# Kernel optimization log

Hardware: AMD Instinct MI355X
Metric: run time of the kernel (lower is better)

## Reference

```python
import jax, jax.numpy as jnp
import numpy as np

C_CONST = 0.0  # polynomial kernel additive constant (init arg c)
D_CONST = 2    # polynomial kernel degree (init arg d)


def setup_inputs() -> dict:
    key = jax.random.key(0)
    k1, k2 = jax.random.split(key)
    input = jax.random.normal(k1, (1, 64, 128, 64), dtype=jnp.float32)
    target = jax.random.normal(k2, (1, 64, 128, 64), dtype=jnp.float32)
    return {"input": input, "target": target}


def reference(input, target):
    ch = input.shape[1]
    hw_input = input.shape[2] * input.shape[3]
    hw_target = target.shape[2] * target.shape[3]
    # Flatten to [hw, c] feature matrices (batch assumed 1, as in the original view(c, -1).T)
    F = input.reshape(ch, -1).T   # [hw_input, c]
    S = target.reshape(ch, -1).T  # [hw_target, c]

    def kernel(A, B):
        # Naive polynomial kernel Gram matrix: (A @ B^T + c)^d
        return (A @ B.T + C_CONST) ** D_CONST

    loss = kernel(F, F) + kernel(S, S) - 2.0 * kernel(F, S)
    return loss.sum() / hw_input / hw_target / (ch ** 2)
```

## Files before the change

### kernel.cpp

```cpp
#include <hip/hip_runtime.h>


#define CH    64
#define KTOT  8192
#define G1    256
#define KPB   (KTOT / G1)
#define KPG   (KPB / 2)

#define NORMF 3.637978807091713e-12f

__global__ __launch_bounds__(512, 4) void gram_partial(
    const float* __restrict__ in, const float* __restrict__ tg,
    float* __restrict__ ws, float* __restrict__ out)
{
    __shared__ __attribute__((aligned(16))) float ts_in[KPB][CH];
    __shared__ __attribute__((aligned(16))) float ts_tg[KPB][CH];
    __shared__ __attribute__((aligned(16))) float red[4096];

    const int t  = threadIdx.x;
    const int k0 = blockIdx.x * KPB;

    if (blockIdx.x == 0 && t == 0) out[0] = 0.f;

    {
        const int lch = t >> 3;
        const int lko = (t & 7) << 2;
        const float4 vi = *(const float4*)(in + lch * KTOT + k0 + lko);
        const float4 vt = *(const float4*)(tg + lch * KTOT + k0 + lko);
        ts_in[lko + 0][lch] = vi.x; ts_in[lko + 1][lch] = vi.y;
        ts_in[lko + 2][lch] = vi.z; ts_in[lko + 3][lch] = vi.w;
        ts_tg[lko + 0][lch] = vt.x; ts_tg[lko + 1][lch] = vt.y;
        ts_tg[lko + 2][lch] = vt.z; ts_tg[lko + 3][lch] = vt.w;
    }
    __syncthreads();

    const int g   = t >> 8;
    const int tid = t & 255;
    const int ty  = tid >> 4;
    const int tx  = tid & 15;
    const int a0  = ty << 2;
    const int b0  = tx << 2;

    float acc[4][4];
#pragma unroll
    for (int i = 0; i < 4; ++i)
#pragma unroll
        for (int j = 0; j < 4; ++j) acc[i][j] = 0.f;

#pragma unroll
    for (int kk = g * KPG; kk < g * KPG + KPG; ++kk) {
        const float4 av = *(const float4*)&ts_in[kk][a0];
        const float4 bv = *(const float4*)&ts_in[kk][b0];
        const float4 cv = *(const float4*)&ts_tg[kk][a0];
        const float4 dv = *(const float4*)&ts_tg[kk][b0];
        const float aa[4] = {av.x, av.y, av.z, av.w};
        const float bb[4] = {bv.x, bv.y, bv.z, bv.w};
        const float cc[4] = {cv.x, cv.y, cv.z, cv.w};
        const float dd[4] = {dv.x, dv.y, dv.z, dv.w};
#pragma unroll
        for (int i = 0; i < 4; ++i)
#pragma unroll
            for (int j = 0; j < 4; ++j) {
                acc[i][j] = fmaf(aa[i], bb[j], acc[i][j]);
                acc[i][j] = fmaf(-cc[i], dd[j], acc[i][j]);
            }
    }

    if (g == 1) {
#pragma unroll
        for (int i = 0; i < 4; ++i) {
            float4 v;
            v.x = acc[i][0]; v.y = acc[i][1]; v.z = acc[i][2]; v.w = acc[i][3];
            *(float4*)&red[tid * 16 + i * 4] = v;
        }
    }
    __syncthreads();
    if (g == 0) {
        float* p = ws + blockIdx.x * 4096;
#pragma unroll
        for (int i = 0; i < 4; ++i) {
            const float4 r = *(const float4*)&red[tid * 16 + i * 4];
            float4 v;
            v.x = acc[i][0] + r.x; v.y = acc[i][1] + r.y;
            v.z = acc[i][2] + r.z; v.w = acc[i][3] + r.w;
            *(float4*)(p + (a0 + i) * 64 + b0) = v;
        }
    }
}

__global__ __launch_bounds__(256) void reduce_square(
    const float* __restrict__ ws, float* __restrict__ out)
{
    __shared__ float red2[4][64];
    const int t  = threadIdx.x;
    const int el = t & 63;
    const int sl = t >> 6;
    const int e  = (blockIdx.x << 6) + el;

    float s = 0.f;
    const int p0 = sl * (G1 / 4);
#pragma unroll 16
    for (int p = p0; p < p0 + (G1 / 4); ++p)
        s += ws[p * 4096 + e];
    red2[sl][el] = s;
    __syncthreads();

    if (t < 64) {
        float tot = red2[0][t] + red2[1][t] + red2[2][t] + red2[3][t];
        float sq  = tot * tot;
#pragma unroll
        for (int off = 32; off > 0; off >>= 1)
            sq += __shfl_down(sq, off);
        if (t == 0) atomicAdd(out, sq * NORMF);
    }
}

extern "C" void kernel_launch(void* const* d_in, const int* in_sizes, int n_in,
                              void* d_out, int out_size, void* d_ws, size_t ws_size,
                              hipStream_t stream)
{
    const float* in = (const float*)d_in[0];
    const float* tg = (const float*)d_in[1];
    float* out = (float*)d_out;
    float* ws  = (float*)d_ws;

    gram_partial<<<G1, 512, 0, stream>>>(in, tg, ws, out);
    reduce_square<<<64, 256, 0, stream>>>(ws, out);
}
```

Before: 62.97 us.

## Use 8x8 register tiles per thread, 4-way K split, and wider reduction grid

The Gram partial kernel now runs 256 threads per block, with each thread computing an 8x8 tile instead of 4x4. Each of the four wavefronts handles 8 of the 32 k-rows, and pairs of wavefronts are combined through an XOR-swizzled shared buffer. This halves the threads per block and increases register reuse per LDS load. Each block now writes two partial 64x64 matrices, so the workspace doubles; the reduce kernel is relaunched with 256 blocks of 16 elements each to read these with more parallelism. The risks are higher register pressure, lower occupancy, and twice as much workspace traffic.

```diff
diff --git a/kernel.cpp b/kernel.cpp
--- a/kernel.cpp
+++ b/kernel.cpp
@@ -4,18 +4,22 @@
 #define CH    64
 #define KTOT  8192
 #define G1    256
-#define KPB   (KTOT / G1)
-#define KPG   (KPB / 2)
+#define KPB   32
+#define KPW   8
+#define NPART 2
+#define NP    (G1 * NPART)
 
 #define NORMF 3.637978807091713e-12f
 
-__global__ __launch_bounds__(512, 4) void gram_partial(
+#define RCOL(row, tb) ((tb) ^ ((row) & 56))
+
+__global__ __launch_bounds__(256, 1) void gram_partial(
     const float* __restrict__ in, const float* __restrict__ tg,
     float* __restrict__ ws, float* __restrict__ out)
 {
     __shared__ __attribute__((aligned(16))) float ts_in[KPB][CH];
     __shared__ __attribute__((aligned(16))) float ts_tg[KPB][CH];
-    __shared__ __attribute__((aligned(16))) float red[4096];
+    __shared__ __attribute__((aligned(16))) float red[2][CH][CH];
 
     const int t  = threadIdx.x;
     const int k0 = blockIdx.x * KPB;
@@ -23,67 +27,82 @@
     if (blockIdx.x == 0 && t == 0) out[0] = 0.f;
 
     {
-        const int lch = t >> 3;
-        const int lko = (t & 7) << 2;
-        const float4 vi = *(const float4*)(in + lch * KTOT + k0 + lko);
-        const float4 vt = *(const float4*)(tg + lch * KTOT + k0 + lko);
-        ts_in[lko + 0][lch] = vi.x; ts_in[lko + 1][lch] = vi.y;
-        ts_in[lko + 2][lch] = vi.z; ts_in[lko + 3][lch] = vi.w;
-        ts_tg[lko + 0][lch] = vt.x; ts_tg[lko + 1][lch] = vt.y;
-        ts_tg[lko + 2][lch] = vt.z; ts_tg[lko + 3][lch] = vt.w;
+        const int lk = (t & 7) << 2;
+#pragma unroll
+        for (int r = 0; r < 2; ++r) {
+            const int lch = (t >> 3) + 32 * r;
+            const float4 vi = *(const float4*)(in + lch * KTOT + k0 + lk);
+            const float4 vt = *(const float4*)(tg + lch * KTOT + k0 + lk);
+            ts_in[lk + 0][lch] = vi.x; ts_in[lk + 1][lch] = vi.y;
+            ts_in[lk + 2][lch] = vi.z; ts_in[lk + 3][lch] = vi.w;
+            ts_tg[lk + 0][lch] = vt.x; ts_tg[lk + 1][lch] = vt.y;
+            ts_tg[lk + 2][lch] = vt.z; ts_tg[lk + 3][lch] = vt.w;
+        }
     }
     __syncthreads();
 
-    const int g   = t >> 8;
-    const int tid = t & 255;
-    const int ty  = tid >> 4;
-    const int tx  = tid & 15;
-    const int a0  = ty << 2;
-    const int b0  = tx << 2;
+    const int w    = t >> 6;
+    const int lane = t & 63;
+    const int ta   = (lane >> 3) << 3;
+    const int tb   = (lane & 7) << 3;
 
-    float acc[4][4];
+    float acc[8][8];
 #pragma unroll
-    for (int i = 0; i < 4; ++i)
+    for (int i = 0; i < 8; ++i)
 #pragma unroll
-        for (int j = 0; j < 4; ++j) acc[i][j] = 0.f;
+        for (int j = 0; j < 8; ++j) acc[i][j] = 0.f;
 
 #pragma unroll
-    for (int kk = g * KPG; kk < g * KPG + KPG; ++kk) {
-        const float4 av = *(const float4*)&ts_in[kk][a0];
-        const float4 bv = *(const float4*)&ts_in[kk][b0];
-        const float4 cv = *(const float4*)&ts_tg[kk][a0];
-        const float4 dv = *(const float4*)&ts_tg[kk][b0];
-        const float aa[4] = {av.x, av.y, av.z, av.w};
-        const float bb[4] = {bv.x, bv.y, bv.z, bv.w};
-        const float cc[4] = {cv.x, cv.y, cv.z, cv.w};
-        const float dd[4] = {dv.x, dv.y, dv.z, dv.w};
+    for (int kk = w * KPW; kk < w * KPW + KPW; ++kk) {
+        const float4 x0 = *(const float4*)&ts_in[kk][ta];
+        const float4 x1 = *(const float4*)&ts_in[kk][ta + 4];
+        const float4 y0 = *(const float4*)&ts_in[kk][tb];
+        const float4 y1 = *(const float4*)&ts_in[kk][tb + 4];
+        const float4 u0 = *(const float4*)&ts_tg[kk][ta];
+        const float4 u1 = *(const float4*)&ts_tg[kk][ta + 4];
+        const float4 v0 = *(const float4*)&ts_tg[kk][tb];
+        const float4 v1 = *(const float4*)&ts_tg[kk][tb + 4];
+        const float A[8] = {x0.x, x0.y, x0.z, x0.w, x1.x, x1.y, x1.z, x1.w};
+        const float B[8] = {y0.x, y0.y, y0.z, y0.w, y1.x, y1.y, y1.z, y1.w};
+        const float C[8] = {u0.x, u0.y, u0.z, u0.w, u1.x, u1.y, u1.z, u1.w};
+        const float D[8] = {v0.x, v0.y, v0.z, v0.w, v1.x, v1.y, v1.z, v1.w};
 #pragma unroll
-        for (int i = 0; i < 4; ++i)
+        for (int i = 0; i < 8; ++i)
 #pragma unroll
-            for (int j = 0; j < 4; ++j) {
-                acc[i][j] = fmaf(aa[i], bb[j], acc[i][j]);
-                acc[i][j] = fmaf(-cc[i], dd[j], acc[i][j]);
+            for (int j = 0; j < 8; ++j) {
+                acc[i][j] = fmaf(A[i], B[j], acc[i][j]);
+                acc[i][j] = fmaf(-C[i], D[j], acc[i][j]);
             }
     }
 
-    if (g == 1) {
+    if (w >= 2) {
 #pragma unroll
-        for (int i = 0; i < 4; ++i) {
-            float4 v;
-            v.x = acc[i][0]; v.y = acc[i][1]; v.z = acc[i][2]; v.w = acc[i][3];
-            *(float4*)&red[tid * 16 + i * 4] = v;
+        for (int i = 0; i < 8; ++i) {
+            const int row = ta + i;
+            const int cc  = RCOL(row, tb);
+            float4 a, b;
+            a.x = acc[i][0]; a.y = acc[i][1]; a.z = acc[i][2]; a.w = acc[i][3];
+            b.x = acc[i][4]; b.y = acc[i][5]; b.z = acc[i][6]; b.w = acc[i][7];
+            *(float4*)&red[w - 2][row][cc]     = a;
+            *(float4*)&red[w - 2][row][cc + 4] = b;
         }
     }
     __syncthreads();
-    if (g == 0) {
-        float* p = ws + blockIdx.x * 4096;
+    if (w < 2) {
+        float* p = ws + (blockIdx.x * NPART + w) * 4096;
 #pragma unroll
-        for (int i = 0; i < 4; ++i) {
-            const float4 r = *(const float4*)&red[tid * 16 + i * 4];
-            float4 v;
-            v.x = acc[i][0] + r.x; v.y = acc[i][1] + r.y;
-            v.z = acc[i][2] + r.z; v.w = acc[i][3] + r.w;
-            *(float4*)(p + (a0 + i) * 64 + b0) = v;
+        for (int i = 0; i < 8; ++i) {
+            const int row = ta + i;
+            const int cc  = RCOL(row, tb);
+            const float4 r0 = *(const float4*)&red[w][row][cc];
+            const float4 r1 = *(const float4*)&red[w][row][cc + 4];
+            float4 a, b;
+            a.x = acc[i][0] + r0.x; a.y = acc[i][1] + r0.y;
+            a.z = acc[i][2] + r0.z; a.w = acc[i][3] + r0.w;
+            b.x = acc[i][4] + r1.x; b.y = acc[i][5] + r1.y;
+            b.z = acc[i][6] + r1.z; b.w = acc[i][7] + r1.w;
+            *(float4*)(p + row * 64 + tb)     = a;
+            *(float4*)(p + row * 64 + tb + 4) = b;
         }
     }
 }
@@ -91,25 +110,30 @@
 __global__ __launch_bounds__(256) void reduce_square(
     const float* __restrict__ ws, float* __restrict__ out)
 {
-    __shared__ float red2[4][64];
+    __shared__ float red2[16][16];
     const int t  = threadIdx.x;
-    const int el = t & 63;
-    const int sl = t >> 6;
-    const int e  = (blockIdx.x << 6) + el;
+    const int el = t & 15;
+    const int sl = t >> 4;
+    const int e  = (blockIdx.x << 4) + el;
 
     float s = 0.f;
-    const int p0 = sl * (G1 / 4);
-#pragma unroll 16
-    for (int p = p0; p < p0 + (G1 / 4); ++p)
+    const int p0 = sl * (NP / 16);
+#pragma unroll
+    for (int p = p0; p < p0 + (NP / 16); ++p)
         s += ws[p * 4096 + e];
     red2[sl][el] = s;
     __syncthreads();
 
     if (t < 64) {
-        float tot = red2[0][t] + red2[1][t] + red2[2][t] + red2[3][t];
-        float sq  = tot * tot;
+        float sq = 0.f;
+        if (t < 16) {
+            float tot = 0.f;
 #pragma unroll
-        for (int off = 32; off > 0; off >>= 1)
+            for (int i = 0; i < 16; ++i) tot += red2[i][t];
+            sq = tot * tot;
+        }
+#pragma unroll
+        for (int off = 8; off > 0; off >>= 1)
             sq += __shfl_down(sq, off);
         if (t == 0) atomicAdd(out, sq * NORMF);
     }
@@ -124,6 +148,6 @@
     float* out = (float*)d_out;
     float* ws  = (float*)d_ws;
 
-    gram_partial<<<G1, 512, 0, stream>>>(in, tg, ws, out);
-    reduce_square<<<64, 256, 0, stream>>>(ws, out);
+    gram_partial<<<G1, 256, 0, stream>>>(in, tg, ws, out);
+    reduce_square<<<256, 256, 0, stream>>>(ws, out);
 }
```

Result: slower. 69.27 us (+10.0%).
